# Optimization experiments

Hardware: AMD Instinct MI355X
Metric: run time of the kernel (lower is better)

## Reference

```python
import jax, jax.numpy as jnp
import numpy as np

T, A, D = 1024, 512, 128
EPS = 1e-5
NEG_SLOPE = 0.01  # torch LeakyReLU default


def setup_inputs() -> dict:
    key = jax.random.key(0)
    ks = jax.random.split(key, 5)
    return {
        "nf_task": jax.random.normal(ks[0], (T, D), dtype=jnp.float32),
        "nf_agent": jax.random.normal(ks[1], (A, D), dtype=jnp.float32),
        "W1": jax.random.normal(ks[2], (D, 2 * D), dtype=jnp.float32) * 0.05,
        "gamma1": jnp.ones((D,), dtype=jnp.float32),
        "beta1": jnp.zeros((D,), dtype=jnp.float32),
        "W2": jax.random.normal(ks[3], (1, D), dtype=jnp.float32) * 0.05,
        "gamma2": jnp.ones((1,), dtype=jnp.float32),
        "beta2": jnp.zeros((1,), dtype=jnp.float32),
        "finished": jax.random.randint(ks[4], (T,), 0, 2, dtype=jnp.int32),
    }


def reference(nf_task, nf_agent, W1, gamma1, beta1, W2, gamma2, beta2, finished):
    d = nf_task.shape[1]
    # Linear(2D->D, no bias) on concat([src, dst]) == src @ W_src^T + dst @ W_dst^T
    src_proj = nf_task @ W1[:, :d].T   # [T, D]
    dst_proj = nf_agent @ W1[:, d:].T  # [A, D]
    h = src_proj[:, None, :] + dst_proj[None, :, :]  # per-edge hidden [T, A, D]
    # BatchNorm1d(D), training mode: batch stats over all edges
    mean = h.mean(axis=(0, 1))
    var = h.var(axis=(0, 1))  # biased, as torch uses for normalization
    h = (h - mean) * jax.lax.rsqrt(var + EPS) * gamma1 + beta1
    # LeakyReLU
    h = jnp.where(h >= 0, h, NEG_SLOPE * h)
    # Linear(D->1, no bias)
    s = jnp.einsum('tad,d->ta', h, W2[0])  # [T, A]
    # BatchNorm1d(1), training mode over all edges
    m2 = s.mean()
    v2 = s.var()
    s = (s - m2) * jax.lax.rsqrt(v2 + EPS) * gamma2[0] + beta2[0]
    # mask edges whose src task is finished
    s = jnp.where(finished.astype(bool)[:, None], -jnp.inf, s)
    # reduce: each agent's mailbox = scores over incoming tasks -> policy [A, T]
    return s.T
```

## Files before the change

kernel.cpp:

```cpp
#include <hip/hip_runtime.h>
#include <math.h>

#define T_N 1024
#define A_N 512
#define D_N 128
#define EPS 1e-5f
#define LDP 132

#define WS_SP   0
#define WS_DP   131072
#define WS_PS   196608
#define WS_SQ   202752
#define WS_S2P  208896
#define WS_S2Q  209408
#define WS_C2   209920
#define WS_F2   209952
#define WS_GO   210464
#define N2F     ((float)(T_N * A_N))

#define MAGIC2 0x2468ACE1u

__device__ __forceinline__ void ast(float* p, float v) {
    __hip_atomic_store(p, v, __ATOMIC_RELAXED, __HIP_MEMORY_SCOPE_AGENT);
}
__device__ __forceinline__ float ald(const float* p) {
    return __hip_atomic_load(p, __ATOMIC_RELAXED, __HIP_MEMORY_SCOPE_AGENT);
}

__global__ __launch_bounds__(256) void ka_proj(const float* __restrict__ task,
                                               const float* __restrict__ agent,
                                               const float* __restrict__ W1,
                                               float* __restrict__ ws)
{
    __shared__ float RT[32 * LDP];
    __shared__ float WT[32 * LDP];
    __shared__ float red[256];
    int b = blockIdx.x, tid = threadIdx.x;
    int rt = b >> 2, ct = b & 3;
    bool is_t = rt < 32;
    const float* src = is_t ? task : agent;
    int woff  = is_t ? 0 : D_N;
    int rbase = (is_t ? rt : rt - 32) * 32;
    int cbase = ct * 32;

    {
        int kq = tid & 31, r0 = tid >> 5;
        for (int i = 0; i < 4; i++) {
            int row = r0 + 8 * i;
            ((float4*)(RT + row * LDP))[kq] = ((const float4*)(src + (rbase + row) * D_N))[kq];
            ((float4*)(WT + row * LDP))[kq] = ((const float4*)(W1 + (cbase + row) * (2 * D_N) + woff))[kq];
        }
    }
    __syncthreads();

    int rg = tid >> 4, cg = tid & 15;
    float a00 = 0, a01 = 0, a10 = 0, a11 = 0;
    for (int kk = 0; kk < 32; kk++) {
        float4 r0 = *(const float4*)(RT + rg * LDP + kk * 4);
        float4 r1 = *(const float4*)(RT + (rg + 16) * LDP + kk * 4);
        float4 w0 = *(const float4*)(WT + cg * LDP + kk * 4);
        float4 w1 = *(const float4*)(WT + (cg + 16) * LDP + kk * 4);
        a00 += r0.x * w0.x + r0.y * w0.y + r0.z * w0.z + r0.w * w0.w;
        a01 += r0.x * w1.x + r0.y * w1.y + r0.z * w1.z + r0.w * w1.w;
        a10 += r1.x * w0.x + r1.y * w0.y + r1.z * w0.z + r1.w * w0.w;
        a11 += r1.x * w1.x + r1.y * w1.y + r1.z * w1.z + r1.w * w1.w;
    }
    float* dst = ws + (is_t ? WS_SP : WS_DP);
    dst[(rbase + rg) * D_N + cbase + cg]           = a00;
    dst[(rbase + rg) * D_N + cbase + cg + 16]      = a01;
    dst[(rbase + rg + 16) * D_N + cbase + cg]      = a10;
    dst[(rbase + rg + 16) * D_N + cbase + cg + 16] = a11;

    float s0 = a00 + a10, s1 = a01 + a11;
    float q0 = a00 * a00 + a10 * a10, q1 = a01 * a01 + a11 * a11;
    for (int off = 16; off <= 32; off <<= 1) {
        s0 += __shfl_xor(s0, off); s1 += __shfl_xor(s1, off);
        q0 += __shfl_xor(q0, off); q1 += __shfl_xor(q1, off);
    }
    int wid = tid >> 6, lane = tid & 63;
    if (lane < 16) {
        red[wid * 64 + lane]      = s0;
        red[wid * 64 + 16 + lane] = s1;
        red[wid * 64 + 32 + lane] = q0;
        red[wid * 64 + 48 + lane] = q1;
    }
    __syncthreads();
    if (tid < 64) {
        float v = red[tid] + red[64 + tid] + red[128 + tid] + red[192 + tid];
        int base = (tid < 32) ? WS_PS : WS_SQ;
        ws[base + rt * 128 + cbase + (tid & 31)] = v;
    }
}

__global__ __launch_bounds__(256) void kb_sweep(const float* __restrict__ g1,
                                                const float* __restrict__ b1,
                                                const float* __restrict__ W2,
                                                const float* __restrict__ g2,
                                                const float* __restrict__ b2,
                                                const int* __restrict__ fin,
                                                float* __restrict__ ws,
                                                float* __restrict__ out)
{
    __shared__ float spT[32 * LDP];
    __shared__ float dpT[32 * LDP];
    __shared__ float scs[128], shs[128];
    __shared__ float stile[32 * 36];
    __shared__ float red[512];

    const int b = blockIdx.x, tid = threadIdx.x;
    const int bx = b & 31, by = b >> 5;
    const int rowbase = bx * 32, colbase = by * 32;
    unsigned* flags = (unsigned*)(ws + WS_F2);
    unsigned* go    = (unsigned*)(ws + WS_GO);

    if (tid < 128) {
        float as = 0.f, ds = 0.f;
        for (int r = 0;  r < 32; r++) as += ws[WS_PS + r * 128 + tid];
        for (int r = 32; r < 48; r++) ds += ws[WS_PS + r * 128 + tid];
        red[tid] = as; red[128 + tid] = ds;
    } else {
        int j = tid - 128;
        float aq = 0.f, dq = 0.f;
        for (int r = 0;  r < 32; r++) aq += ws[WS_SQ + r * 128 + j];
        for (int r = 32; r < 48; r++) dq += ws[WS_SQ + r * 128 + j];
        red[256 + j] = aq; red[384 + j] = dq;
    }
    __syncthreads();
    if (tid < 128) {
        float ms = red[tid] * (1.f / T_N);
        float md = red[128 + tid] * (1.f / A_N);
        float var = red[256 + tid] * (1.f / T_N) - ms * ms
                  + red[384 + tid] * (1.f / A_N) - md * md;
        float s = g1[tid] * rsqrtf(var + EPS);
        scs[tid] = s;
        shs[tid] = b1[tid] - (ms + md) * s;
    }
    __syncthreads();

    {
        int k = (tid & 31) * 4, r8 = tid >> 5;
        float4 sc4 = *(const float4*)(scs + k);
        float4 sh4 = *(const float4*)(shs + k);
        for (int it = 0; it < 4; it++) {
            int t = it * 8 + r8;
            float4 v = *(const float4*)(ws + WS_SP + (rowbase + t) * D_N + k);
            v.x *= sc4.x; v.y *= sc4.y; v.z *= sc4.z; v.w *= sc4.w;
            *(float4*)(spT + t * LDP + k) = v;
        }
        for (int it = 0; it < 4; it++) {
            int a = it * 8 + r8;
            float4 v = *(const float4*)(ws + WS_DP + (colbase + a) * D_N + k);
            v.x = v.x * sc4.x + sh4.x; v.y = v.y * sc4.y + sh4.y;
            v.z = v.z * sc4.z + sh4.z; v.w = v.w * sc4.w + sh4.w;
            *(float4*)(dpT + a * LDP + k) = v;
        }
    }
    __syncthreads();

    int tx = tid & 15, ty = tid >> 4;
    float a00 = 0, a01 = 0, a10 = 0, a11 = 0;
    #pragma unroll 4
    for (int kk = 0; kk < 32; kk++) {
        float4 wv = *(const float4*)(W2 + kk * 4);
        float w5x = 0.505f * wv.x, w5y = 0.505f * wv.y, w5z = 0.505f * wv.z, w5w = 0.505f * wv.w;
        float w9x = 0.495f * wv.x, w9y = 0.495f * wv.y, w9z = 0.495f * wv.z, w9w = 0.495f * wv.w;
        float4 s0 = *(const float4*)(spT + ty * LDP + kk * 4);
        float4 s1 = *(const float4*)(spT + (ty + 16) * LDP + kk * 4);
        float4 d0 = *(const float4*)(dpT + tx * LDP + kk * 4);
        float4 d1 = *(const float4*)(dpT + (tx + 16) * LDP + kk * 4);
        float u;
        u = s0.x + d0.x; a00 = fmaf(w5x, u, a00); a00 = fmaf(w9x, fabsf(u), a00);
        u = s0.y + d0.y; a00 = fmaf(w5y, u, a00); a00 = fmaf(w9y, fabsf(u), a00);
        u = s0.z + d0.z; a00 = fmaf(w5z, u, a00); a00 = fmaf(w9z, fabsf(u), a00);
        u = s0.w + d0.w; a00 = fmaf(w5w, u, a00); a00 = fmaf(w9w, fabsf(u), a00);
        u = s0.x + d1.x; a01 = fmaf(w5x, u, a01); a01 = fmaf(w9x, fabsf(u), a01);
        u = s0.y + d1.y; a01 = fmaf(w5y, u, a01); a01 = fmaf(w9y, fabsf(u), a01);
        u = s0.z + d1.z; a01 = fmaf(w5z, u, a01); a01 = fmaf(w9z, fabsf(u), a01);
        u = s0.w + d1.w; a01 = fmaf(w5w, u, a01); a01 = fmaf(w9w, fabsf(u), a01);
        u = s1.x + d0.x; a10 = fmaf(w5x, u, a10); a10 = fmaf(w9x, fabsf(u), a10);
        u = s1.y + d0.y; a10 = fmaf(w5y, u, a10); a10 = fmaf(w9y, fabsf(u), a10);
        u = s1.z + d0.z; a10 = fmaf(w5z, u, a10); a10 = fmaf(w9z, fabsf(u), a10);
        u = s1.w + d0.w; a10 = fmaf(w5w, u, a10); a10 = fmaf(w9w, fabsf(u), a10);
        u = s1.x + d1.x; a11 = fmaf(w5x, u, a11); a11 = fmaf(w9x, fabsf(u), a11);
        u = s1.y + d1.y; a11 = fmaf(w5y, u, a11); a11 = fmaf(w9y, fabsf(u), a11);
        u = s1.z + d1.z; a11 = fmaf(w5z, u, a11); a11 = fmaf(w9z, fabsf(u), a11);
        u = s1.w + d1.w; a11 = fmaf(w5w, u, a11); a11 = fmaf(w9w, fabsf(u), a11);
    }

    {
        float lsum = a00 + a01 + a10 + a11;
        float lsq  = a00 * a00 + a01 * a01 + a10 * a10 + a11 * a11;
        stile[tx * 36 + ty]              = a00;
        stile[(tx + 16) * 36 + ty]       = a01;
        stile[tx * 36 + ty + 16]         = a10;
        stile[(tx + 16) * 36 + ty + 16]  = a11;
        for (int off = 1; off <= 32; off <<= 1) {
            lsum += __shfl_xor(lsum, off);
            lsq  += __shfl_xor(lsq,  off);
        }
        int wid = tid >> 6;
        if ((tid & 63) == 0) { red[wid] = lsum; red[8 + wid] = lsq; }
        __syncthreads();
        if (tid == 0) {
            ast(ws + WS_S2P + b, red[0] + red[1] + red[2] + red[3]);
            ast(ws + WS_S2Q + b, red[8] + red[9] + red[10] + red[11]);
        }
    }

    __syncthreads();
    if (tid == 0)
        __hip_atomic_store(&flags[b], MAGIC2, __ATOMIC_RELAXED, __HIP_MEMORY_SCOPE_AGENT);
    if (b == 0) {
        while (__hip_atomic_load(&flags[tid], __ATOMIC_RELAXED, __HIP_MEMORY_SCOPE_AGENT) != MAGIC2 ||
               __hip_atomic_load(&flags[tid + 256], __ATOMIC_RELAXED, __HIP_MEMORY_SCOPE_AGENT) != MAGIC2)
            __builtin_amdgcn_s_sleep(1);
        __syncthreads();
        float v1 = ald(ws + WS_S2P + tid) + ald(ws + WS_S2P + 256 + tid);
        float v2 = ald(ws + WS_S2Q + tid) + ald(ws + WS_S2Q + 256 + tid);
        for (int off = 1; off <= 32; off <<= 1) {
            v1 += __shfl_xor(v1, off);
            v2 += __shfl_xor(v2, off);
        }
        if ((tid & 63) == 0) { red[tid >> 6] = v1; red[8 + (tid >> 6)] = v2; }
        __syncthreads();
        if (tid == 0) {
            float s2s = red[0] + red[1] + red[2] + red[3];
            float s2q = red[8] + red[9] + red[10] + red[11];
            float m2   = s2s / N2F;
            float var2 = s2q / N2F - m2 * m2;
            float sc2 = g2[0] * rsqrtf(var2 + EPS);
            ast(ws + WS_C2,     sc2);
            ast(ws + WS_C2 + 1, b2[0] - m2 * sc2);
            __hip_atomic_store(go, MAGIC2, __ATOMIC_RELEASE, __HIP_MEMORY_SCOPE_AGENT);
        }
    }
    if (tid == 0)
        while (__hip_atomic_load(go, __ATOMIC_RELAXED, __HIP_MEMORY_SCOPE_AGENT) != MAGIC2)
            __builtin_amdgcn_s_sleep(8);
    __syncthreads();

    {
        if (tid == 0) { red[0] = ald(ws + WS_C2); red[1] = ald(ws + WS_C2 + 1); }
        __syncthreads();
        float sc2 = red[0], sh2 = red[1];
        const float NEG = -1.0e38f;
        int j4 = (tid & 7) * 4, a = tid >> 3;
        int4 f = *(const int4*)(fin + rowbase + j4);
        float4 v = *(const float4*)(stile + a * 36 + j4);
        float4 o;
        o.x = f.x ? NEG : v.x * sc2 + sh2;
        o.y = f.y ? NEG : v.y * sc2 + sh2;
        o.z = f.z ? NEG : v.z * sc2 + sh2;
        o.w = f.w ? NEG : v.w * sc2 + sh2;
        *(float4*)(out + (colbase + a) * T_N + rowbase + j4) = o;
    }
}

extern "C" void kernel_launch(void* const* d_in, const int* in_sizes, int n_in,
                              void* d_out, int out_size, void* d_ws, size_t ws_size,
                              hipStream_t stream) {
    (void)in_sizes; (void)n_in; (void)out_size; (void)ws_size;
    const float* task  = (const float*)d_in[0];
    const float* agent = (const float*)d_in[1];
    const float* W1    = (const float*)d_in[2];
    const float* g1    = (const float*)d_in[3];
    const float* b1    = (const float*)d_in[4];
    const float* W2    = (const float*)d_in[5];
    const float* g2    = (const float*)d_in[6];
    const float* b2    = (const float*)d_in[7];
    const int*   fin   = (const int*)d_in[8];

    ka_proj<<<192, 256, 0, stream>>>(task, agent, W1, (float*)d_ws);
    kb_sweep<<<512, 256, 0, stream>>>(g1, b1, W2, g2, b2, fin, (float*)d_ws, (float*)d_out);
}
```

Before: 87.98 us.

## Split D across waves with 4x4 register tiles and k-major smem layout

Restructures the per-block edge sweep so each of the four waves handles a quarter of the hidden dimension with a 4x4 register tile over a 32x32 edge tile. The sp/dp tiles are stored transposed (k-major, padded stride 33), which allows float4 loads across edges. The four partial sums are then accumulated through shared memory in a serialized pass. The global loads of the projections are also issued before the BN1 statistics reduction to hide their latency, and the spin-wait sleep is shortened. The cost is a four-step serialized stile accumulation with extra barriers, and scalar transposed smem stores that may cause bank conflicts.

New measurement: 93.53 us. +6.3%, slower.

```diff
diff --git a/kernel.cpp b/kernel.cpp
--- a/kernel.cpp
+++ b/kernel.cpp
@@ -6,6 +6,7 @@
 #define D_N 128
 #define EPS 1e-5f
 #define LDP 132
+#define TSP 33
 
 #define WS_SP   0
 #define WS_DP   131072
@@ -101,8 +102,8 @@
                                                 float* __restrict__ ws,
                                                 float* __restrict__ out)
 {
-    __shared__ float spT[32 * LDP];
-    __shared__ float dpT[32 * LDP];
+    __shared__ float spT[128 * TSP];
+    __shared__ float dpT[128 * TSP];
     __shared__ float scs[128], shs[128];
     __shared__ float stile[32 * 36];
     __shared__ float red[512];
@@ -112,6 +113,13 @@
     const int rowbase = bx * 32, colbase = by * 32;
     unsigned* flags = (unsigned*)(ws + WS_F2);
     unsigned* go    = (unsigned*)(ws + WS_GO);
+
+    const int kq = tid & 31, r8 = tid >> 5;
+    float4 sraw[4], draw[4];
+    for (int it = 0; it < 4; it++) {
+        sraw[it] = *(const float4*)(ws + WS_SP + (rowbase + it * 8 + r8) * D_N + kq * 4);
+        draw[it] = *(const float4*)(ws + WS_DP + (colbase + it * 8 + r8) * D_N + kq * 4);
+    }
 
     if (tid < 128) {
         float as = 0.f, ds = 0.f;
@@ -138,62 +146,74 @@
     __syncthreads();
 
     {
-        int k = (tid & 31) * 4, r8 = tid >> 5;
-        float4 sc4 = *(const float4*)(scs + k);
-        float4 sh4 = *(const float4*)(shs + k);
+        float4 sc4 = *(const float4*)(scs + kq * 4);
+        float4 sh4 = *(const float4*)(shs + kq * 4);
         for (int it = 0; it < 4; it++) {
             int t = it * 8 + r8;
-            float4 v = *(const float4*)(ws + WS_SP + (rowbase + t) * D_N + k);
-            v.x *= sc4.x; v.y *= sc4.y; v.z *= sc4.z; v.w *= sc4.w;
-            *(float4*)(spT + t * LDP + k) = v;
-        }
-        for (int it = 0; it < 4; it++) {
-            int a = it * 8 + r8;
-            float4 v = *(const float4*)(ws + WS_DP + (colbase + a) * D_N + k);
-            v.x = v.x * sc4.x + sh4.x; v.y = v.y * sc4.y + sh4.y;
-            v.z = v.z * sc4.z + sh4.z; v.w = v.w * sc4.w + sh4.w;
-            *(float4*)(dpT + a * LDP + k) = v;
-        }
-    }
-    __syncthreads();
-
-    int tx = tid & 15, ty = tid >> 4;
-    float a00 = 0, a01 = 0, a10 = 0, a11 = 0;
-    #pragma unroll 4
-    for (int kk = 0; kk < 32; kk++) {
-        float4 wv = *(const float4*)(W2 + kk * 4);
-        float w5x = 0.505f * wv.x, w5y = 0.505f * wv.y, w5z = 0.505f * wv.z, w5w = 0.505f * wv.w;
-        float w9x = 0.495f * wv.x, w9y = 0.495f * wv.y, w9z = 0.495f * wv.z, w9w = 0.495f * wv.w;
-        float4 s0 = *(const float4*)(spT + ty * LDP + kk * 4);
-        float4 s1 = *(const float4*)(spT + (ty + 16) * LDP + kk * 4);
-        float4 d0 = *(const float4*)(dpT + tx * LDP + kk * 4);
-        float4 d1 = *(const float4*)(dpT + (tx + 16) * LDP + kk * 4);
-        float u;
-        u = s0.x + d0.x; a00 = fmaf(w5x, u, a00); a00 = fmaf(w9x, fabsf(u), a00);
-        u = s0.y + d0.y; a00 = fmaf(w5y, u, a00); a00 = fmaf(w9y, fabsf(u), a00);
-        u = s0.z + d0.z; a00 = fmaf(w5z, u, a00); a00 = fmaf(w9z, fabsf(u), a00);
-        u = s0.w + d0.w; a00 = fmaf(w5w, u, a00); a00 = fmaf(w9w, fabsf(u), a00);
-        u = s0.x + d1.x; a01 = fmaf(w5x, u, a01); a01 = fmaf(w9x, fabsf(u), a01);
-        u = s0.y + d1.y; a01 = fmaf(w5y, u, a01); a01 = fmaf(w9y, fabsf(u), a01);
-        u = s0.z + d1.z; a01 = fmaf(w5z, u, a01); a01 = fmaf(w9z, fabsf(u), a01);
-        u = s0.w + d1.w; a01 = fmaf(w5w, u, a01); a01 = fmaf(w9w, fabsf(u), a01);
-        u = s1.x + d0.x; a10 = fmaf(w5x, u, a10); a10 = fmaf(w9x, fabsf(u), a10);
-        u = s1.y + d0.y; a10 = fmaf(w5y, u, a10); a10 = fmaf(w9y, fabsf(u), a10);
-        u = s1.z + d0.z; a10 = fmaf(w5z, u, a10); a10 = fmaf(w9z, fabsf(u), a10);
-        u = s1.w + d0.w; a10 = fmaf(w5w, u, a10); a10 = fmaf(w9w, fabsf(u), a10);
-        u = s1.x + d1.x; a11 = fmaf(w5x, u, a11); a11 = fmaf(w9x, fabsf(u), a11);
-        u = s1.y + d1.y; a11 = fmaf(w5y, u, a11); a11 = fmaf(w9y, fabsf(u), a11);
-        u = s1.z + d1.z; a11 = fmaf(w5z, u, a11); a11 = fmaf(w9z, fabsf(u), a11);
-        u = s1.w + d1.w; a11 = fmaf(w5w, u, a11); a11 = fmaf(w9w, fabsf(u), a11);
-    }
-
-    {
-        float lsum = a00 + a01 + a10 + a11;
-        float lsq  = a00 * a00 + a01 * a01 + a10 * a10 + a11 * a11;
-        stile[tx * 36 + ty]              = a00;
-        stile[(tx + 16) * 36 + ty]       = a01;
-        stile[tx * 36 + ty + 16]         = a10;
-        stile[(tx + 16) * 36 + ty + 16]  = a11;
+            float4 v = sraw[it];
+            spT[(kq * 4 + 0) * TSP + t] = v.x * sc4.x;
+            spT[(kq * 4 + 1) * TSP + t] = v.y * sc4.y;
+            spT[(kq * 4 + 2) * TSP + t] = v.z * sc4.z;
+            spT[(kq * 4 + 3) * TSP + t] = v.w * sc4.w;
+            float4 w = draw[it];
+            dpT[(kq * 4 + 0) * TSP + t] = w.x * sc4.x + sh4.x;
+            dpT[(kq * 4 + 1) * TSP + t] = w.y * sc4.y + sh4.y;
+            dpT[(kq * 4 + 2) * TSP + t] = w.z * sc4.z + sh4.z;
+            dpT[(kq * 4 + 3) * TSP + t] = w.w * sc4.w + sh4.w;
+        }
+    }
+    __syncthreads();
+
+    const int kg = tid >> 6, lane = tid & 63;
+    const int ty = lane >> 3, tx = lane & 7;
+    float acc[4][4] = {};
+    {
+        const float* spk = spT + (kg * 32) * TSP + ty * 4;
+        const float* dpk = dpT + (kg * 32) * TSP + tx * 4;
+        const float* w2k = W2 + kg * 32;
+        #pragma unroll 8
+        for (int k = 0; k < 32; k++) {
+            float wv = w2k[k];
+            float w5 = 0.505f * wv, w9 = 0.495f * wv;
+            float4 sv = *(const float4*)(spk + k * TSP);
+            float4 dv = *(const float4*)(dpk + k * TSP);
+            float u;
+            u = sv.x + dv.x; acc[0][0] = fmaf(w5, u, acc[0][0]); acc[0][0] = fmaf(w9, fabsf(u), acc[0][0]);
+            u = sv.x + dv.y; acc[0][1] = fmaf(w5, u, acc[0][1]); acc[0][1] = fmaf(w9, fabsf(u), acc[0][1]);
+            u = sv.x + dv.z; acc[0][2] = fmaf(w5, u, acc[0][2]); acc[0][2] = fmaf(w9, fabsf(u), acc[0][2]);
+            u = sv.x + dv.w; acc[0][3] = fmaf(w5, u, acc[0][3]); acc[0][3] = fmaf(w9, fabsf(u), acc[0][3]);
+            u = sv.y + dv.x; acc[1][0] = fmaf(w5, u, acc[1][0]); acc[1][0] = fmaf(w9, fabsf(u), acc[1][0]);
+            u = sv.y + dv.y; acc[1][1] = fmaf(w5, u, acc[1][1]); acc[1][1] = fmaf(w9, fabsf(u), acc[1][1]);
+            u = sv.y + dv.z; acc[1][2] = fmaf(w5, u, acc[1][2]); acc[1][2] = fmaf(w9, fabsf(u), acc[1][2]);
+            u = sv.y + dv.w; acc[1][3] = fmaf(w5, u, acc[1][3]); acc[1][3] = fmaf(w9, fabsf(u), acc[1][3]);
+            u = sv.z + dv.x; acc[2][0] = fmaf(w5, u, acc[2][0]); acc[2][0] = fmaf(w9, fabsf(u), acc[2][0]);
+            u = sv.z + dv.y; acc[2][1] = fmaf(w5, u, acc[2][1]); acc[2][1] = fmaf(w9, fabsf(u), acc[2][1]);
+            u = sv.z + dv.z; acc[2][2] = fmaf(w5, u, acc[2][2]); acc[2][2] = fmaf(w9, fabsf(u), acc[2][2]);
+            u = sv.z + dv.w; acc[2][3] = fmaf(w5, u, acc[2][3]); acc[2][3] = fmaf(w9, fabsf(u), acc[2][3]);
+            u = sv.w + dv.x; acc[3][0] = fmaf(w5, u, acc[3][0]); acc[3][0] = fmaf(w9, fabsf(u), acc[3][0]);
+            u = sv.w + dv.y; acc[3][1] = fmaf(w5, u, acc[3][1]); acc[3][1] = fmaf(w9, fabsf(u), acc[3][1]);
+            u = sv.w + dv.z; acc[3][2] = fmaf(w5, u, acc[3][2]); acc[3][2] = fmaf(w9, fabsf(u), acc[3][2]);
+            u = sv.w + dv.w; acc[3][3] = fmaf(w5, u, acc[3][3]); acc[3][3] = fmaf(w9, fabsf(u), acc[3][3]);
+        }
+    }
+
+    for (int g = 0; g < 4; g++) {
+        if (kg == g) {
+            for (int i = 0; i < 4; i++)
+                for (int j = 0; j < 4; j++) {
+                    int idx = (tx * 4 + j) * 36 + ty * 4 + i;
+                    if (g == 0) stile[idx] = acc[i][j];
+                    else        stile[idx] += acc[i][j];
+                }
+        }
+        __syncthreads();
+    }
+
+    {
+        int a = tid >> 3, t4 = (tid & 7) * 4;
+        float4 v = *(const float4*)(stile + a * 36 + t4);
+        float lsum = v.x + v.y + v.z + v.w;
+        float lsq  = v.x * v.x + v.y * v.y + v.z * v.z + v.w * v.w;
         for (int off = 1; off <= 32; off <<= 1) {
             lsum += __shfl_xor(lsum, off);
             lsq  += __shfl_xor(lsq,  off);
@@ -236,7 +256,7 @@
     }
     if (tid == 0)
         while (__hip_atomic_load(go, __ATOMIC_RELAXED, __HIP_MEMORY_SCOPE_AGENT) != MAGIC2)
-            __builtin_amdgcn_s_sleep(8);
+            __builtin_amdgcn_s_sleep(4);
     __syncthreads();
 
     {
```
